# Kernel tuning notes

Hardware: AMD Instinct MI355X
Metric: run time of the kernel (lower is better)

## Reference

```python
import jax, jax.numpy as jnp
import numpy as np

MINVAL = 0.0
MAXVAL = 1.0


def setup_inputs() -> dict:
    key = jax.random.key(0)
    k1, k2, k3, k4 = jax.random.split(key, 4)
    B, C, G = 16, 16, 4096
    density = jax.random.uniform(k1, (B, 1, G), dtype=jnp.float32)
    xi = jax.random.uniform(k2, (C - 1,), dtype=jnp.float32, minval=-1.0, maxval=1.0)
    grid = jnp.sort(jax.random.uniform(k3, (G,), dtype=jnp.float32))
    grid_weights = jax.random.uniform(k4, (G,), dtype=jnp.float32)
    return {"density": density, "xi": xi, "grid": grid, "grid_weights": grid_weights}


def reference(density, xi, grid, grid_weights):
    # xi -> positive length scales via sigmoid reparameterization
    xi_t = 1.0 / (MINVAL + (MAXVAL - MINVAL) * jax.nn.sigmoid(xi))  # (C-1,)
    # pairwise squared distances on the grid: (G, G)
    g = (grid[:, None] - grid[None, :]) ** 2
    # per-channel Gaussian kernel: (C-1, G, G)
    expo = jnp.exp(-g[None, :, :] * xi_t[:, None, None]) * (0.5 * xi_t[:, None, None])
    # weighted density contracted against each channel kernel: (B, C-1, G)
    integral = jnp.einsum('jkl,ilm->jim', density * grid_weights, expo)
    # append raw density as the last channel: (B, C, G)
    return jnp.concatenate([integral, density], axis=1)
```

## Files before the change

kernel.cpp:

```cpp
#include <hip/hip_runtime.h>
#include <hip/hip_bf16.h>
#include <math.h>


#define RTERMS 24
#define NC 32
#define LOG2E 1.4426950408889634f

__global__ void gcl_moments(const float* __restrict__ density, const float* __restrict__ xi,
                            const float* __restrict__ grid, const float* __restrict__ gw,
                            float* __restrict__ ws, int G) {
    int i = blockIdx.x;
    int c = blockIdx.y;
    int t = threadIdx.x;
    int b = t >> 4;
    int s = t & 15;
    float xt = 1.0f + __expf(-xi[i]);
    float a = -xt * LOG2E;

    float acc[RTERMS];
#pragma unroll
    for (int n = 0; n < RTERMS; ++n) acc[n] = 0.0f;

    int chunk = G / NC;
    int l0 = c * chunk;
    int iters = chunk >> 4;
    for (int it = 0; it < iters; ++it) {
        int l = l0 + it * 16 + s;
        float gl = grid[l];
        float w = density[b * G + l] * gw[l] * exp2f(a * gl * gl);
        float gl2 = gl * gl;
        float gl4 = gl2 * gl2;
        float p0 = w, p1 = w * gl, p2 = w * gl2, p3 = w * gl2 * gl;
#pragma unroll
        for (int k = 0; k < RTERMS / 4; ++k) {
            acc[4 * k + 0] += p0; p0 *= gl4;
            acc[4 * k + 1] += p1; p1 *= gl4;
            acc[4 * k + 2] += p2; p2 *= gl4;
            acc[4 * k + 3] += p3; p3 *= gl4;
        }
    }

#pragma unroll
    for (int n = 0; n < RTERMS; ++n) {
        float v = acc[n];
        v += __shfl_xor(v, 1, 16);
        v += __shfl_xor(v, 2, 16);
        v += __shfl_xor(v, 4, 16);
        v += __shfl_xor(v, 8, 16);
        acc[n] = v;
    }
    if (s == 0) {
        float* base = ws + ((size_t)(i * NC + c) * RTERMS) * 16 + b;
#pragma unroll
        for (int n = 0; n < RTERMS; ++n) base[n * 16] = acc[n];
    }
}

__global__ void gcl_eval(const float* __restrict__ density, const float* __restrict__ xi,
                         const float* __restrict__ grid, const float* __restrict__ ws,
                         float* __restrict__ out, int G, int CH) {
    int i = blockIdx.y;
    int b = blockIdx.z;
    int m = blockIdx.x * blockDim.x + threadIdx.x;
    int C = CH + 1;
    if (i == CH) {
        out[((size_t)b * C + i) * G + m] = density[b * G + m];
        return;
    }
    float xt = 1.0f + __expf(-xi[i]);
    float a = -xt * LOG2E;

    __shared__ float T[RTERMS];
    if (threadIdx.x < RTERMS) {
        const float invfact[RTERMS] = {
            1.0f, 1.0f, 0.5f, 1.6666667e-1f, 4.1666667e-2f, 8.3333333e-3f,
            1.3888889e-3f, 1.9841270e-4f, 2.4801587e-5f, 2.7557319e-6f,
            2.7557319e-7f, 2.5052108e-8f, 2.0876757e-9f, 1.6059044e-10f,
            1.1470746e-11f, 7.6471637e-13f, 4.7794773e-14f, 2.8114573e-15f,
            1.5619207e-16f, 8.2206352e-18f, 4.1103176e-19f, 1.9572941e-20f,
            8.8967914e-22f, 3.8681702e-23f};
        int n = threadIdx.x;
        float cf = exp2f((float)n * __log2f(2.0f * xt)) * invfact[n];
        const float* p = ws + ((size_t)(i * NC) * RTERMS + n) * 16 + b;
        float ssum = 0.0f;
#pragma unroll
        for (int cc = 0; cc < NC; ++cc) ssum += p[(size_t)cc * RTERMS * 16];
        T[n] = cf * ssum;
    }
    __syncthreads();

    float gm = grid[m];
    float g2 = gm * gm;
    float he = T[RTERMS - 2], ho = T[RTERMS - 1];
#pragma unroll
    for (int k = RTERMS - 4; k >= 0; k -= 2) {
        he = he * g2 + T[k];
        ho = ho * g2 + T[k + 1];
    }
    out[((size_t)b * C + i) * G + m] = exp2f(a * g2) * (0.5f * xt) * (he + gm * ho);
}

extern "C" void kernel_launch(void* const* d_in, const int* in_sizes, int n_in,
                              void* d_out, int out_size, void* d_ws, size_t ws_size,
                              hipStream_t stream) {
    const float* density = (const float*)d_in[0];
    const float* xi      = (const float*)d_in[1];
    const float* grid    = (const float*)d_in[2];
    const float* gw      = (const float*)d_in[3];
    float* out = (float*)d_out;
    float* ws  = (float*)d_ws;

    int CH = in_sizes[1];
    int G  = in_sizes[2];
    int B  = in_sizes[0] / G;

    gcl_moments<<<dim3(CH, NC), 256, 0, stream>>>(density, xi, grid, gw, ws, G);
    gcl_eval<<<dim3(G / 256, CH + 1, B), 256, 0, stream>>>(density, xi, grid, ws, out, G, CH);
}
```

Baseline: 73.87 us.

## Fuse moment and evaluation kernels into one per (channel,batch) block

```diff
diff --git a/kernel.cpp b/kernel.cpp
--- a/kernel.cpp
+++ b/kernel.cpp
@@ -4,17 +4,24 @@
 
 
 #define RTERMS 24
-#define NC 32
 #define LOG2E 1.4426950408889634f
 
-__global__ void gcl_moments(const float* __restrict__ density, const float* __restrict__ xi,
-                            const float* __restrict__ grid, const float* __restrict__ gw,
-                            float* __restrict__ ws, int G) {
+__global__ __launch_bounds__(256) void gcl_fused(
+        const float* __restrict__ density, const float* __restrict__ xi,
+        const float* __restrict__ grid, const float* __restrict__ gw,
+        float* __restrict__ out, int G, int CH) {
     int i = blockIdx.x;
-    int c = blockIdx.y;
+    int b = blockIdx.y;
+    int C = CH + 1;
     int t = threadIdx.x;
-    int b = t >> 4;
-    int s = t & 15;
+
+    if (i == CH) {
+        const float4* src = (const float4*)(density + (size_t)b * G);
+        float4* dst = (float4*)(out + ((size_t)b * C + CH) * G);
+        for (int j = t; j < G / 4; j += 256) dst[j] = src[j];
+        return;
+    }
+
     float xt = 1.0f + __expf(-xi[i]);
     float a = -xt * LOG2E;
 
@@ -22,16 +29,14 @@
 #pragma unroll
     for (int n = 0; n < RTERMS; ++n) acc[n] = 0.0f;
 
-    int chunk = G / NC;
-    int l0 = c * chunk;
-    int iters = chunk >> 4;
+    const float* drow = density + (size_t)b * G;
+    int iters = G >> 8;
     for (int it = 0; it < iters; ++it) {
-        int l = l0 + it * 16 + s;
+        int l = (it << 8) + t;
         float gl = grid[l];
-        float w = density[b * G + l] * gw[l] * exp2f(a * gl * gl);
-        float gl2 = gl * gl;
-        float gl4 = gl2 * gl2;
-        float p0 = w, p1 = w * gl, p2 = w * gl2, p3 = w * gl2 * gl;
+        float w = drow[l] * gw[l] * exp2f(a * gl * gl);
+        float gl2 = gl * gl, gl4 = gl2 * gl2;
+        float p0 = w, p1 = w * gl, p2 = w * gl2, p3 = p2 * gl;
 #pragma unroll
         for (int k = 0; k < RTERMS / 4; ++k) {
             acc[4 * k + 0] += p0; p0 *= gl4;
@@ -44,35 +49,23 @@
 #pragma unroll
     for (int n = 0; n < RTERMS; ++n) {
         float v = acc[n];
-        v += __shfl_xor(v, 1, 16);
-        v += __shfl_xor(v, 2, 16);
-        v += __shfl_xor(v, 4, 16);
-        v += __shfl_xor(v, 8, 16);
+        v += __shfl_xor(v, 1);
+        v += __shfl_xor(v, 2);
+        v += __shfl_xor(v, 4);
+        v += __shfl_xor(v, 8);
+        v += __shfl_xor(v, 16);
+        v += __shfl_xor(v, 32);
         acc[n] = v;
     }
-    if (s == 0) {
-        float* base = ws + ((size_t)(i * NC + c) * RTERMS) * 16 + b;
+    __shared__ float part[4][RTERMS];
+    __shared__ float T[RTERMS];
+    int wave = t >> 6, lane = t & 63;
+    if (lane == 0) {
 #pragma unroll
-        for (int n = 0; n < RTERMS; ++n) base[n * 16] = acc[n];
+        for (int n = 0; n < RTERMS; ++n) part[wave][n] = acc[n];
     }
-}
-
-__global__ void gcl_eval(const float* __restrict__ density, const float* __restrict__ xi,
-                         const float* __restrict__ grid, const float* __restrict__ ws,
-                         float* __restrict__ out, int G, int CH) {
-    int i = blockIdx.y;
-    int b = blockIdx.z;
-    int m = blockIdx.x * blockDim.x + threadIdx.x;
-    int C = CH + 1;
-    if (i == CH) {
-        out[((size_t)b * C + i) * G + m] = density[b * G + m];
-        return;
-    }
-    float xt = 1.0f + __expf(-xi[i]);
-    float a = -xt * LOG2E;
-
-    __shared__ float T[RTERMS];
-    if (threadIdx.x < RTERMS) {
+    __syncthreads();
+    if (t < RTERMS) {
         const float invfact[RTERMS] = {
             1.0f, 1.0f, 0.5f, 1.6666667e-1f, 4.1666667e-2f, 8.3333333e-3f,
             1.3888889e-3f, 1.9841270e-4f, 2.4801587e-5f, 2.7557319e-6f,
@@ -80,25 +73,30 @@
             1.1470746e-11f, 7.6471637e-13f, 4.7794773e-14f, 2.8114573e-15f,
             1.5619207e-16f, 8.2206352e-18f, 4.1103176e-19f, 1.9572941e-20f,
             8.8967914e-22f, 3.8681702e-23f};
-        int n = threadIdx.x;
-        float cf = exp2f((float)n * __log2f(2.0f * xt)) * invfact[n];
-        const float* p = ws + ((size_t)(i * NC) * RTERMS + n) * 16 + b;
-        float ssum = 0.0f;
-#pragma unroll
-        for (int cc = 0; cc < NC; ++cc) ssum += p[(size_t)cc * RTERMS * 16];
-        T[n] = cf * ssum;
+        float s = part[0][t] + part[1][t] + part[2][t] + part[3][t];
+        float cf = exp2f((float)t * __log2f(2.0f * xt)) * invfact[t];
+        T[t] = s * cf;
     }
     __syncthreads();
 
-    float gm = grid[m];
-    float g2 = gm * gm;
-    float he = T[RTERMS - 2], ho = T[RTERMS - 1];
+    float Tr[RTERMS];
 #pragma unroll
-    for (int k = RTERMS - 4; k >= 0; k -= 2) {
-        he = he * g2 + T[k];
-        ho = ho * g2 + T[k + 1];
+    for (int n = 0; n < RTERMS; ++n) Tr[n] = T[n];
+
+    float sc = 0.5f * xt;
+    float* orow = out + ((size_t)b * C + i) * G;
+    for (int it = 0; it < iters; ++it) {
+        int m = (it << 8) + t;
+        float gm = grid[m];
+        float g2 = gm * gm;
+        float he = Tr[RTERMS - 2], ho = Tr[RTERMS - 1];
+#pragma unroll
+        for (int k = RTERMS - 4; k >= 0; k -= 2) {
+            he = he * g2 + Tr[k];
+            ho = ho * g2 + Tr[k + 1];
+        }
+        orow[m] = exp2f(a * g2) * sc * (he + gm * ho);
     }
-    out[((size_t)b * C + i) * G + m] = exp2f(a * g2) * (0.5f * xt) * (he + gm * ho);
 }
 
 extern "C" void kernel_launch(void* const* d_in, const int* in_sizes, int n_in,
@@ -109,12 +107,10 @@
     const float* grid    = (const float*)d_in[2];
     const float* gw      = (const float*)d_in[3];
     float* out = (float*)d_out;
-    float* ws  = (float*)d_ws;
 
     int CH = in_sizes[1];
     int G  = in_sizes[2];
     int B  = in_sizes[0] / G;
 
-    gcl_moments<<<dim3(CH, NC), 256, 0, stream>>>(density, xi, grid, gw, ws, G);
-    gcl_eval<<<dim3(G / 256, CH + 1, B), 256, 0, stream>>>(density, xi, grid, ws, out, G, CH);
+    gcl_fused<<<dim3(CH + 1, B), 256, 0, stream>>>(density, xi, grid, gw, out, G, CH);
 }
```

Measured after the change: 71.18 us. -3.6%, faster.
